# Optimization experiments

Hardware: AMD Instinct MI355X
Metric: run time of the kernel (lower is better)

The kernel has to match this reference:

```python
import jax, jax.numpy as jnp
import numpy as np

B, S, D = 2, 2048, 1024
H, DH = 16, 64  # H*DH == D


def setup_inputs() -> dict:
    key = jax.random.key(0)
    ks = jax.random.split(key, 7)
    scale = 1.0 / np.sqrt(D)
    return {
        "x": jax.random.normal(ks[0], (B, S, D), dtype=jnp.float32),
        "mask": jax.random.normal(ks[1], (B, 1, 1, S), dtype=jnp.float32),
        "Wq": jax.random.normal(ks[2], (D, D), dtype=jnp.float32) * scale,
        "Wk": jax.random.normal(ks[3], (D, D), dtype=jnp.float32) * scale,
        "Wv": jax.random.normal(ks[4], (D, D), dtype=jnp.float32) * scale,
        "Wo": jax.random.normal(ks[5], (D, D), dtype=jnp.float32) * scale,
        "bo": jax.random.normal(ks[6], (D,), dtype=jnp.float32) * 0.01,
    }


def reference(x, mask, Wq, Wk, Wv, Wo, bo):
    # QKV projections (bias-free), split heads: [B,S,D] -> [B,H,S,DH]
    def split_heads(t):
        return t.reshape(B, S, H, DH).transpose(0, 2, 1, 3)

    q = split_heads(x @ Wq)
    k = split_heads(x @ Wk)
    v = split_heads(x @ Wv)

    # NOTE: module scales by sqrt(input_dim), not sqrt(head_size)
    scores = jnp.einsum("bhqd,bhkd->bhqk", q, k) / jnp.sqrt(jnp.float32(D))
    scores = scores + mask  # additive mask, broadcast [B,1,1,S]
    attn = jax.nn.softmax(scores, axis=-1)
    ctx = jnp.einsum("bhqk,bhkd->bhqd", attn, v)  # [B,H,S,DH]
    ctx = ctx.transpose(0, 2, 1, 3).reshape(B, S, H * DH)
    return ctx @ Wo + bo
```

## Files before the change

### kernel.cpp

```cpp
#include <hip/hip_runtime.h>
#include <hip/hip_bf16.h>

#define BB 2
#define SS 2048
#define DD 1024
#define HH 16
#define DHD 64
#define QKLD 2048

typedef __attribute__((ext_vector_type(8))) __bf16 bf16x8;
typedef __attribute__((ext_vector_type(4))) __bf16 bf16x4;
typedef __attribute__((ext_vector_type(4))) float f32x4;

__device__ __forceinline__ f32x4 mfma16(bf16x8 a, bf16x8 b, f32x4 c) {
  return __builtin_amdgcn_mfma_f32_16x16x32_bf16(a, b, c, 0, 0, 0);
}
__device__ __forceinline__ void gload_lds16(const void* g, void* l) {
  __builtin_amdgcn_global_load_lds((__attribute__((address_space(1))) const void*)g,
                                   (__attribute__((address_space(3))) void*)l, 16, 0, 0);
}

__global__ __launch_bounds__(256) void prep_kernel(
    const float* __restrict__ x, __bf16* __restrict__ xb,
    const float* __restrict__ mask, __bf16* __restrict__ embf,
    const float* __restrict__ Wq, const float* __restrict__ Wk,
    const float* __restrict__ Wv, const float* __restrict__ Wo,
    __bf16* __restrict__ WTbase) {
  __shared__ __bf16 t[64][65];
  int id = blockIdx.x, tid = threadIdx.x;
  if (id < 4096) {
    int i = id * 256 + tid;
    float4 f = ((const float4*)x)[i];
    bf16x4 o;
    o[0] = (__bf16)f.x; o[1] = (__bf16)f.y; o[2] = (__bf16)f.z; o[3] = (__bf16)f.w;
    *(bf16x4*)(xb + (size_t)i * 4) = o;
    return;
  }
  if (id < 4112) {
    int j = (id - 4096) * 256 + tid;
    embf[j] = (__bf16)__expf(mask[j]);
    return;
  }
  int idx = id - 4112;
  int z = idx >> 8, rem = idx & 255;
  const float* W = (z == 0) ? Wq : (z == 1) ? Wk : (z == 2) ? Wv : Wo;
  __bf16* WT = WTbase + ((size_t)z << 20);
  int c0 = (rem & 15) * 64, r0 = (rem >> 4) * 64;
  {
    int rr = tid >> 4, cg = tid & 15;
#pragma unroll
    for (int it = 0; it < 4; ++it) {
      int r = rr + it * 16;
      float4 f = *(const float4*)(W + (size_t)(r0 + r) * DD + c0 + cg * 4);
      t[r][cg * 4 + 0] = (__bf16)f.x;
      t[r][cg * 4 + 1] = (__bf16)f.y;
      t[r][cg * 4 + 2] = (__bf16)f.z;
      t[r][cg * 4 + 3] = (__bf16)f.w;
    }
  }
  __syncthreads();
  {
    int sg = tid & 7;
#pragma unroll
    for (int it = 0; it < 2; ++it) {
      int wc = (tid >> 3) + it * 32;
      __bf16 tmp[8];
#pragma unroll
      for (int e = 0; e < 8; ++e) tmp[e] = t[sg * 8 + e][wc];
      bf16x8 o;
#pragma unroll
      for (int e = 0; e < 8; ++e) o[e] = tmp[e];
      *(bf16x8*)(WT + (size_t)(c0 + wc) * DD + r0 + sg * 8) = o;
    }
  }
}

template <int MODE>
__device__ __forceinline__ void gemm_body(
    char* AsB, char* BsB, int bx, int by,
    const __bf16* __restrict__ A, const __bf16* __restrict__ BT,
    float* __restrict__ Cf, __bf16* __restrict__ Cb,
    const float* __restrict__ bias, const __bf16* __restrict__ embf,
    int M, int N, int K) {
  int tid = threadIdx.x;
  int lane = tid & 63, wave = tid >> 6;
  int lr = lane & 15, lg = lane >> 4;
  int wr = wave >> 1, wc = wave & 1;
  int m0 = bx * 128, n0 = by * 128;

  int o0 = wave * 1024 + lane * 16;
  int r0i = o0 >> 6, s0i = ((o0 >> 4) & 3) ^ (r0i & 3);
  int o1 = o0 + 4096;
  int r1i = o1 >> 6, s1i = ((o1 >> 4) & 3) ^ (r1i & 3);

  const __bf16* Ag0 = A + (size_t)(m0 + r0i) * K + s0i * 8;
  const __bf16* Ag1 = A + (size_t)(m0 + r1i) * K + s1i * 8;
  const __bf16* Bg0 = BT + (size_t)(n0 + r0i) * K + s0i * 8;
  const __bf16* Bg1 = BT + (size_t)(n0 + r1i) * K + s1i * 8;
  int lb0 = wave * 1024, lb1 = wave * 1024 + 4096;

  f32x4 acc[4][4];
#pragma unroll
  for (int m = 0; m < 4; ++m)
#pragma unroll
    for (int n = 0; n < 4; ++n) acc[m][n] = (f32x4){0.f, 0.f, 0.f, 0.f};

  gload_lds16(Ag0, AsB + lb0);
  gload_lds16(Ag1, AsB + lb1);
  gload_lds16(Bg0, BsB + lb0);
  gload_lds16(Bg1, BsB + lb1);
  __syncthreads();

  int NK = K >> 5;
  for (int it = 0; it < NK; ++it) {
    int cur = it & 1;
    if (it + 1 < NK) {
      int ko = (it + 1) * 32;
      char* An = AsB + (cur ^ 1) * 8192;
      char* Bn = BsB + (cur ^ 1) * 8192;
      gload_lds16(Ag0 + ko, An + lb0);
      gload_lds16(Ag1 + ko, An + lb1);
      gload_lds16(Bg0 + ko, Bn + lb0);
      gload_lds16(Bg1 + ko, Bn + lb1);
    }
    const char* Ab = AsB + cur * 8192;
    const char* Bb = BsB + cur * 8192;
    bf16x8 af[4], bfr[4];
#pragma unroll
    for (int m = 0; m < 4; ++m) {
      int row = wr * 64 + m * 16 + lr;
      af[m] = *(const bf16x8*)(Ab + row * 64 + ((lg ^ (row & 3)) << 4));
    }
#pragma unroll
    for (int n = 0; n < 4; ++n) {
      int row = wc * 64 + n * 16 + lr;
      bfr[n] = *(const bf16x8*)(Bb + row * 64 + ((lg ^ (row & 3)) << 4));
    }
#pragma unroll
    for (int m = 0; m < 4; ++m)
#pragma unroll
      for (int n = 0; n < 4; ++n) acc[m][n] = mfma16(af[m], bfr[n], acc[m][n]);
    __syncthreads();
  }

#pragma unroll
  for (int m = 0; m < 4; ++m) {
#pragma unroll
    for (int n = 0; n < 4; ++n) {
      int cc = n0 + wc * 64 + n * 16 + lr;
      float ef = 0.f;
      if constexpr (MODE == 2) ef = (float)embf[cc];
#pragma unroll
      for (int r = 0; r < 4; ++r) {
        int rr = m0 + wr * 64 + m * 16 + 4 * lg + r;
        if constexpr (MODE == 1) {
          Cf[(size_t)rr * N + cc] = acc[m][n][r] + bias[cc];
        } else if constexpr (MODE == 0) {
          Cb[(size_t)rr * N + cc] = (__bf16)acc[m][n][r];
        } else {
          int bb2 = cc >> 11, sl = cc & (SS - 1);
          int hh = rr >> 6, dd2 = rr & 63;
          Cb[(((size_t)bb2 * HH + hh) * DHD + dd2) * SS + sl] =
              (__bf16)(acc[m][n][r] * ef);
        }
      }
    }
  }
}

__global__ __launch_bounds__(256, 2) void proj_kernel(
    const __bf16* __restrict__ xb, const __bf16* __restrict__ WqT,
    const __bf16* __restrict__ WvT, __bf16* __restrict__ qkb,
    __bf16* __restrict__ vtb, const __bf16* __restrict__ embf) {
  __shared__ __bf16 As[2][128 * 32];
  __shared__ __bf16 Bs[2][128 * 32];
  int id = blockIdx.x;
  if (id < 512) {
    gemm_body<0>((char*)As, (char*)Bs, id & 31, id >> 5,
                 xb, WqT, nullptr, qkb, nullptr, nullptr, 4096, 2048, 1024);
  } else {
    int i2 = id - 512;
    gemm_body<2>((char*)As, (char*)Bs, i2 & 7, i2 >> 3,
                 WvT, xb, nullptr, vtb, nullptr, embf, 1024, 4096, 1024);
  }
}

__global__ __launch_bounds__(256, 2) void ogemm_kernel(
    const __bf16* __restrict__ ctxb, const __bf16* __restrict__ WoT,
    float* __restrict__ out, const float* __restrict__ bo) {
  __shared__ __bf16 As[2][128 * 32];
  __shared__ __bf16 Bs[2][128 * 32];
  gemm_body<1>((char*)As, (char*)Bs, blockIdx.x, blockIdx.y,
               ctxb, WoT, out, nullptr, bo, nullptr, 4096, 1024, 1024);
}

__global__ __launch_bounds__(512, 4) void attn_kernel(
    const __bf16* __restrict__ QK, const __bf16* __restrict__ VT,
    const __bf16* __restrict__ embf, __bf16* __restrict__ ctxb) {
  __shared__ __bf16 Ks[2][64 * 64];
  __shared__ __bf16 Vs[2][64 * 64];
  __shared__ __attribute__((aligned(16))) __bf16 pS[8][16][72];

  int h = blockIdx.y, b = blockIdx.z;
  int tid = threadIdx.x;
  int wave = tid >> 6, lane = tid & 63;
  int lr = lane & 15, lg = lane >> 4;

  int q0 = blockIdx.x * 128 + wave * 16;
  const __bf16* qp = QK + ((size_t)(b * SS) + q0 + lr) * QKLD + h * DHD;
  bf16x8 qa[2];
#pragma unroll
  for (int kc = 0; kc < 2; ++kc)
    qa[kc] = *(const bf16x8*)(qp + kc * 32 + 8 * lg);

  int o0 = tid * 16;
  int row0 = o0 >> 7;
  int ss0 = ((o0 >> 4) & 7) ^ (row0 & 7);
  int lw = wave * 1024;

  const __bf16* kg = QK + (size_t)(b * SS) * QKLD + DD + h * DHD;
  const __bf16* vg = VT + ((size_t)(b * HH + h) * DHD) * SS;
  const __bf16* Kg0 = kg + (size_t)row0 * QKLD + ss0 * 8;
  const __bf16* Vg0 = vg + (size_t)row0 * SS + ss0 * 8;
  const __bf16* ep = embf + b * SS + 8 * lg;

  gload_lds16(Kg0, (char*)Ks[0] + lw);
  gload_lds16(Vg0, (char*)Vs[0] + lw);

  f32x4 ctx[4], lacc;
  lacc = (f32x4){0.f, 0.f, 0.f, 0.f};
#pragma unroll
  for (int c = 0; c < 4; ++c) ctx[c] = (f32x4){0.f, 0.f, 0.f, 0.f};
  const float SCALE = 0.03125f;
  __syncthreads();

  const int NT = SS / 64;
  for (int it = 0; it < NT; ++it) {
    int cur = it & 1;
    int kb = it * 64;
    if (it + 1 < NT) {
      size_t ko = (size_t)(it + 1) * 64 * QKLD;
      int vo = (it + 1) * 64;
      gload_lds16(Kg0 + ko, (char*)Ks[cur ^ 1] + lw);
      gload_lds16(Vg0 + vo, (char*)Vs[cur ^ 1] + lw);
    }
    const char* Kb = (const char*)Ks[cur];
    const char* Vb = (const char*)Vs[cur];
    f32x4 s[4];
#pragma unroll
    for (int f = 0; f < 4; ++f) s[f] = (f32x4){0.f, 0.f, 0.f, 0.f};
#pragma unroll
    for (int f = 0; f < 4; ++f) {
      int row = f * 16 + lr;
#pragma unroll
      for (int kc = 0; kc < 2; ++kc) {
        bf16x8 kf = *(const bf16x8*)(Kb + row * 128 + (((kc * 4 + lg) ^ (row & 7)) << 4));
        s[f] = mfma16(qa[kc], kf, s[f]);
      }
    }
#pragma unroll
    for (int f = 0; f < 4; ++f)
#pragma unroll
      for (int r = 0; r < 4; ++r)
        pS[wave][4 * lg + r][f * 16 + lr] = (__bf16)__expf(s[f][r] * SCALE);
    bf16x8 emf[2];
    emf[0] = *(const bf16x8*)(ep + kb);
    emf[1] = *(const bf16x8*)(ep + kb + 32);
    bf16x8 pa[2];
#pragma unroll
    for (int kc = 0; kc < 2; ++kc)
      pa[kc] = *(const bf16x8*)(&pS[wave][lr][kc * 32 + 8 * lg]);
    lacc = mfma16(pa[0], emf[0], lacc);
    lacc = mfma16(pa[1], emf[1], lacc);
#pragma unroll
    for (int c = 0; c < 4; ++c) {
      int row = c * 16 + lr;
#pragma unroll
      for (int kc = 0; kc < 2; ++kc) {
        bf16x8 vf = *(const bf16x8*)(Vb + row * 128 + (((kc * 4 + lg) ^ (row & 7)) << 4));
        ctx[c] = mfma16(pa[kc], vf, ctx[c]);
      }
    }
    __syncthreads();
  }
  __bf16* op = ctxb + ((size_t)(b * SS) + q0 + 4 * lg) * DD + h * DHD + lr;
#pragma unroll
  for (int r = 0; r < 4; ++r) {
    float inv = 1.0f / lacc[r];
#pragma unroll
    for (int c = 0; c < 4; ++c)
      op[(size_t)r * DD + c * 16] = (__bf16)(ctx[c][r] * inv);
  }
}

extern "C" void kernel_launch(void* const* d_in, const int* in_sizes, int n_in,
                              void* d_out, int out_size, void* d_ws, size_t ws_size,
                              hipStream_t stream) {
  const float* x    = (const float*)d_in[0];
  const float* mask = (const float*)d_in[1];
  const float* Wq   = (const float*)d_in[2];
  const float* Wk   = (const float*)d_in[3];
  const float* Wv   = (const float*)d_in[4];
  const float* Wo   = (const float*)d_in[5];
  const float* bo   = (const float*)d_in[6];
  float* out = (float*)d_out;

  char* ws = (char*)d_ws;
  const size_t MB = 1024 * 1024;
  __bf16* xb   = (__bf16*)(ws + 0);
  __bf16* WqT  = (__bf16*)(ws + 8 * MB);
  __bf16* WvT  = (__bf16*)(ws + 12 * MB);
  __bf16* WoT  = (__bf16*)(ws + 14 * MB);
  __bf16* qkb  = (__bf16*)(ws + 16 * MB);
  __bf16* vtb  = (__bf16*)(ws + 32 * MB);
  __bf16* embf = (__bf16*)(ws + 40 * MB);
  __bf16* ctxb = xb;

  prep_kernel<<<5136, 256, 0, stream>>>(x, xb, mask, embf, Wq, Wk, Wv, Wo, WqT);
  proj_kernel<<<768, 256, 0, stream>>>(xb, WqT, WvT, qkb, vtb, embf);
  attn_kernel<<<dim3(16, HH, BB), 512, 0, stream>>>(qkb, vtb, embf, ctxb);
  ogemm_kernel<<<dim3(32, 8), 256, 0, stream>>>(ctxb, WoT, out, bo);
}
```

Baseline: 212.9 us.

## Rewrite attention with 32x32x16 MFMA and register-resident probabilities

The attention kernel moves from 16x16x32 MFMA tiles to 32x32x16 tiles, with 4 waves each handling 32 query rows instead of 8 waves of 16 rows. Scores are computed transposed (K as the A operand), so the exponentiated probabilities can be packed and exchanged across half-waves with shuffles. This replaces the round trip through the per-wave LDS pS buffer. The aim is to cut LDS traffic and improve MFMA efficiency, at the cost of more registers per thread and fewer waves per block.

```diff
diff --git a/kernel.cpp b/kernel.cpp
--- a/kernel.cpp
+++ b/kernel.cpp
@@ -11,13 +11,33 @@
 typedef __attribute__((ext_vector_type(8))) __bf16 bf16x8;
 typedef __attribute__((ext_vector_type(4))) __bf16 bf16x4;
 typedef __attribute__((ext_vector_type(4))) float f32x4;
+typedef __attribute__((ext_vector_type(16))) float f32x16;
 
 __device__ __forceinline__ f32x4 mfma16(bf16x8 a, bf16x8 b, f32x4 c) {
   return __builtin_amdgcn_mfma_f32_16x16x32_bf16(a, b, c, 0, 0, 0);
+}
+__device__ __forceinline__ f32x16 mfma32(bf16x8 a, bf16x8 b, f32x16 c) {
+  return __builtin_amdgcn_mfma_f32_32x32x16_bf16(a, b, c, 0, 0, 0);
 }
 __device__ __forceinline__ void gload_lds16(const void* g, void* l) {
   __builtin_amdgcn_global_load_lds((__attribute__((address_space(1))) const void*)g,
                                    (__attribute__((address_space(3))) void*)l, 16, 0, 0);
+}
+__device__ __forceinline__ f32x16 zero16() {
+  f32x16 z;
+#pragma unroll
+  for (int i = 0; i < 16; ++i) z[i] = 0.f;
+  return z;
+}
+__device__ __forceinline__ bf16x8 frag4(unsigned a, unsigned b, unsigned c, unsigned d) {
+  union { unsigned u[4]; bf16x8 v; } x;
+  x.u[0] = a; x.u[1] = b; x.u[2] = c; x.u[3] = d;
+  return x.v;
+}
+__device__ __forceinline__ unsigned pack2(float lo, float hi) {
+  union { __bf16 h[2]; unsigned u; } x;
+  x.h[0] = (__bf16)lo; x.h[1] = (__bf16)hi;
+  return x.u;
 }
 
 __global__ __launch_bounds__(256) void prep_kernel(
@@ -194,43 +214,43 @@
                ctxb, WoT, out, nullptr, bo, nullptr, 4096, 1024, 1024);
 }
 
-__global__ __launch_bounds__(512, 4) void attn_kernel(
+__global__ __launch_bounds__(256, 2) void attn_kernel(
     const __bf16* __restrict__ QK, const __bf16* __restrict__ VT,
     const __bf16* __restrict__ embf, __bf16* __restrict__ ctxb) {
   __shared__ __bf16 Ks[2][64 * 64];
   __shared__ __bf16 Vs[2][64 * 64];
-  __shared__ __attribute__((aligned(16))) __bf16 pS[8][16][72];
 
   int h = blockIdx.y, b = blockIdx.z;
   int tid = threadIdx.x;
   int wave = tid >> 6, lane = tid & 63;
-  int lr = lane & 15, lg = lane >> 4;
-
-  int q0 = blockIdx.x * 128 + wave * 16;
-  const __bf16* qp = QK + ((size_t)(b * SS) + q0 + lr) * QKLD + h * DHD;
-  bf16x8 qa[2];
-#pragma unroll
-  for (int kc = 0; kc < 2; ++kc)
-    qa[kc] = *(const bf16x8*)(qp + kc * 32 + 8 * lg);
+  int l31 = lane & 31, hi = lane >> 5;
+  int rx = l31 & 7;
+
+  int q0 = blockIdx.x * 128 + wave * 32;
+  const __bf16* qp = QK + ((size_t)(b * SS) + q0 + l31) * QKLD + h * DHD + 8 * hi;
+  bf16x8 qfrag[4];
+#pragma unroll
+  for (int kc = 0; kc < 4; ++kc) qfrag[kc] = *(const bf16x8*)(qp + 16 * kc);
 
   int o0 = tid * 16;
   int row0 = o0 >> 7;
   int ss0 = ((o0 >> 4) & 7) ^ (row0 & 7);
-  int lw = wave * 1024;
+  int lw0 = wave * 1024, lw1 = wave * 1024 + 4096;
 
   const __bf16* kg = QK + (size_t)(b * SS) * QKLD + DD + h * DHD;
   const __bf16* vg = VT + ((size_t)(b * HH + h) * DHD) * SS;
   const __bf16* Kg0 = kg + (size_t)row0 * QKLD + ss0 * 8;
+  const __bf16* Kg1 = kg + (size_t)(row0 + 32) * QKLD + ss0 * 8;
   const __bf16* Vg0 = vg + (size_t)row0 * SS + ss0 * 8;
-  const __bf16* ep = embf + b * SS + 8 * lg;
-
-  gload_lds16(Kg0, (char*)Ks[0] + lw);
-  gload_lds16(Vg0, (char*)Vs[0] + lw);
-
-  f32x4 ctx[4], lacc;
-  lacc = (f32x4){0.f, 0.f, 0.f, 0.f};
-#pragma unroll
-  for (int c = 0; c < 4; ++c) ctx[c] = (f32x4){0.f, 0.f, 0.f, 0.f};
+  const __bf16* Vg1 = vg + (size_t)(row0 + 32) * SS + ss0 * 8;
+  const __bf16* ep = embf + b * SS + 8 * hi;
+
+  gload_lds16(Kg0, (char*)Ks[0] + lw0);
+  gload_lds16(Kg1, (char*)Ks[0] + lw1);
+  gload_lds16(Vg0, (char*)Vs[0] + lw0);
+  gload_lds16(Vg1, (char*)Vs[0] + lw1);
+
+  f32x16 ctx0 = zero16(), ctx1 = zero16(), lacc = zero16();
   const float SCALE = 0.03125f;
   __syncthreads();
 
@@ -241,55 +261,70 @@
     if (it + 1 < NT) {
       size_t ko = (size_t)(it + 1) * 64 * QKLD;
       int vo = (it + 1) * 64;
-      gload_lds16(Kg0 + ko, (char*)Ks[cur ^ 1] + lw);
-      gload_lds16(Vg0 + vo, (char*)Vs[cur ^ 1] + lw);
-    }
+      gload_lds16(Kg0 + ko, (char*)Ks[cur ^ 1] + lw0);
+      gload_lds16(Kg1 + ko, (char*)Ks[cur ^ 1] + lw1);
+      gload_lds16(Vg0 + vo, (char*)Vs[cur ^ 1] + lw0);
+      gload_lds16(Vg1 + vo, (char*)Vs[cur ^ 1] + lw1);
+    }
+    bf16x8 emf[4];
+#pragma unroll
+    for (int q2 = 0; q2 < 4; ++q2) emf[q2] = *(const bf16x8*)(ep + kb + 16 * q2);
+
     const char* Kb = (const char*)Ks[cur];
     const char* Vb = (const char*)Vs[cur];
-    f32x4 s[4];
-#pragma unroll
-    for (int f = 0; f < 4; ++f) s[f] = (f32x4){0.f, 0.f, 0.f, 0.f};
-#pragma unroll
-    for (int f = 0; f < 4; ++f) {
-      int row = f * 16 + lr;
-#pragma unroll
-      for (int kc = 0; kc < 2; ++kc) {
-        bf16x8 kf = *(const bf16x8*)(Kb + row * 128 + (((kc * 4 + lg) ^ (row & 7)) << 4));
-        s[f] = mfma16(qa[kc], kf, s[f]);
+#pragma unroll
+    for (int kc32 = 0; kc32 < 2; ++kc32) {
+      f32x16 sc = zero16();
+#pragma unroll
+      for (int kc = 0; kc < 4; ++kc) {
+        bf16x8 kf = *(const bf16x8*)(Kb + (kc32 * 32 + l31) * 128 +
+                                     ((((kc << 1) + hi) ^ rx) << 4));
+        sc = mfma32(kf, qfrag[kc], sc);
       }
-    }
-#pragma unroll
-    for (int f = 0; f < 4; ++f)
-#pragma unroll
-      for (int r = 0; r < 4; ++r)
-        pS[wave][4 * lg + r][f * 16 + lr] = (__bf16)__expf(s[f][r] * SCALE);
-    bf16x8 emf[2];
-    emf[0] = *(const bf16x8*)(ep + kb);
-    emf[1] = *(const bf16x8*)(ep + kb + 32);
-    bf16x8 pa[2];
-#pragma unroll
-    for (int kc = 0; kc < 2; ++kc)
-      pa[kc] = *(const bf16x8*)(&pS[wave][lr][kc * 32 + 8 * lg]);
-    lacc = mfma16(pa[0], emf[0], lacc);
-    lacc = mfma16(pa[1], emf[1], lacc);
-#pragma unroll
-    for (int c = 0; c < 4; ++c) {
-      int row = c * 16 + lr;
-#pragma unroll
-      for (int kc = 0; kc < 2; ++kc) {
-        bf16x8 vf = *(const bf16x8*)(Vb + row * 128 + (((kc * 4 + lg) ^ (row & 7)) << 4));
-        ctx[c] = mfma16(pa[kc], vf, ctx[c]);
+      unsigned pk[8];
+#pragma unroll
+      for (int i2 = 0; i2 < 8; ++i2)
+        pk[i2] = pack2(__expf(sc[2 * i2] * SCALE), __expf(sc[2 * i2 + 1] * SCALE));
+      unsigned sx0 = __shfl_xor(pk[0], 32, 64);
+      unsigned sx1 = __shfl_xor(pk[1], 32, 64);
+      unsigned sx2 = __shfl_xor(pk[2], 32, 64);
+      unsigned sx3 = __shfl_xor(pk[3], 32, 64);
+      unsigned sx4 = __shfl_xor(pk[4], 32, 64);
+      unsigned sx5 = __shfl_xor(pk[5], 32, 64);
+      unsigned sx6 = __shfl_xor(pk[6], 32, 64);
+      unsigned sx7 = __shfl_xor(pk[7], 32, 64);
+      unsigned w0 = hi ? sx2 : pk[0];
+      unsigned w1 = hi ? sx3 : pk[1];
+      unsigned w2 = hi ? pk[2] : sx0;
+      unsigned w3 = hi ? pk[3] : sx1;
+      unsigned w4 = hi ? sx6 : pk[4];
+      unsigned w5 = hi ? sx7 : pk[5];
+      unsigned w6 = hi ? pk[6] : sx4;
+      unsigned w7 = hi ? pk[7] : sx5;
+      bf16x8 pf0 = frag4(w0, w1, w2, w3);
+      bf16x8 pf1 = frag4(w4, w5, w6, w7);
+      lacc = mfma32(pf0, emf[kc32 * 2 + 0], lacc);
+      lacc = mfma32(pf1, emf[kc32 * 2 + 1], lacc);
+      {
+        bf16x8 v00 = *(const bf16x8*)(Vb + (l31)*128 + ((((kc32 << 2) + 0 + hi) ^ rx) << 4));
+        ctx0 = mfma32(pf0, v00, ctx0);
+        bf16x8 v01 = *(const bf16x8*)(Vb + (l31)*128 + ((((kc32 << 2) + 2 + hi) ^ rx) << 4));
+        ctx0 = mfma32(pf1, v01, ctx0);
+        bf16x8 v10 = *(const bf16x8*)(Vb + (32 + l31) * 128 + ((((kc32 << 2) + 0 + hi) ^ rx) << 4));
+        ctx1 = mfma32(pf0, v10, ctx1);
+        bf16x8 v11 = *(const bf16x8*)(Vb + (32 + l31) * 128 + ((((kc32 << 2) + 2 + hi) ^ rx) << 4));
+        ctx1 = mfma32(pf1, v11, ctx1);
       }
     }
     __syncthreads();
   }
-  __bf16* op = ctxb + ((size_t)(b * SS) + q0 + 4 * lg) * DD + h * DHD + lr;
-#pragma unroll
-  for (int r = 0; r < 4; ++r) {
-    float inv = 1.0f / lacc[r];
-#pragma unroll
-    for (int c = 0; c < 4; ++c)
-      op[(size_t)r * DD + c * 16] = (__bf16)(ctx[c][r] * inv);
+#pragma unroll
+  for (int i = 0; i < 16; ++i) {
+    float inv = 1.0f / lacc[i];
+    int q = (i & 3) + 8 * (i >> 2) + 4 * hi;
+    __bf16* op = ctxb + ((size_t)(b * SS) + q0 + q) * DD + h * DHD + l31;
+    op[0] = (__bf16)(ctx0[i] * inv);
+    op[32] = (__bf16)(ctx1[i] * inv);
   }
 }
 
@@ -318,6 +353,6 @@
 
   prep_kernel<<<5136, 256, 0, stream>>>(x, xb, mask, embf, Wq, Wk, Wv, Wo, WqT);
   proj_kernel<<<768, 256, 0, stream>>>(xb, WqT, WvT, qkb, vtb, embf);
-  attn_kernel<<<dim3(16, HH, BB), 512, 0, stream>>>(qkb, vtb, embf, ctxb);
+  attn_kernel<<<dim3(16, HH, BB), 256, 0, stream>>>(qkb, vtb, embf, ctxb);
   ogemm_kernel<<<dim3(32, 8), 256, 0, stream>>>(ctxb, WoT, out, bo);
 }
```

Result: no change. 208.9 us (-1.9%).
